# Kernel optimization log

Hardware: AMD Instinct MI355X
Metric: run time of the kernel (lower is better)

The kernel has to match this reference:

```python
import jax, jax.numpy as jnp
import numpy as np

N = 512       # num_nodes (feature dim of x == num_nodes, per GCNConv(num_nodes, f1))
BZ = 32       # subjects
TC = 256      # tc_length
F1 = 256
F2 = 128
E = 524288    # edges in the given (corr) graph over all bz*N nodes
NTOT = BZ * N
SLOPE = 0.2   # leaky relu negative_slope


def setup_inputs() -> dict:
    key = jax.random.key(0)
    ks = jax.random.split(key, 17)
    w = lambda k, shape: (jax.random.normal(k, shape, jnp.float32) * (shape[-1] ** -0.5))
    return {
        "x": jax.random.normal(ks[0], (NTOT, N), jnp.float32),
        "t": jax.random.normal(ks[1], (NTOT, TC), jnp.float32),
        "gumbel_u": jax.random.uniform(ks[2], (BZ, N, N, 2), jnp.float32),
        "edge_index": jax.random.randint(ks[3], (2, E), 0, NTOT, jnp.int64 if jax.config.jax_enable_x64 else jnp.int32),
        "conv1_w": w(ks[4], (F1, N)),
        "conv1_b": jnp.zeros((F1,), jnp.float32),
        "conv2_w": w(ks[5], (F2, F1)),
        "conv2_b": jnp.zeros((F2,), jnp.float32),
        "fc_cat_w": w(ks[6], (2, 2 * TC)),
        "fc_cat_b": jnp.zeros((2,), jnp.float32),
        "fcn1_w": w(ks[7], (256, F2 * 2 * N)),
        "fcn1_b": jnp.zeros((256,), jnp.float32),
        "fcn2_w": w(ks[8], (32, 256)),
        "fcn2_b": jnp.zeros((32,), jnp.float32),
        "fcn3_w": w(ks[9], (2, 32)),
        "fcn3_b": jnp.zeros((2,), jnp.float32),
    }


def _gcn_dense(x, A, W, b):
    # PyG GCNConv on a dense 0/1 adjacency A (edge r->c means A[r,c]=1):
    # add self loop, in-degree symmetric norm, aggregate sources into targets.
    n = A.shape[0]
    Ah = A + jnp.eye(n, dtype=A.dtype)
    deg = Ah.sum(axis=0)                                  # in-degree (targets = cols)
    dis = jnp.where(deg > 0, jax.lax.rsqrt(deg), 0.0)
    M = dis[:, None] * Ah * dis[None, :]                  # M[j,i] = d_j^-1/2 A_hat[j,i] d_i^-1/2
    return M.T @ (x @ W.T) + b


def _gcn_sparse(x, row, col, W, b):
    n = x.shape[0]
    loops = jnp.arange(n, dtype=row.dtype)
    r = jnp.concatenate([row, loops])
    c = jnp.concatenate([col, loops])
    deg = jax.ops.segment_sum(jnp.ones_like(c, x.dtype), c, num_segments=n)
    dis = jnp.where(deg > 0, jax.lax.rsqrt(deg), 0.0)
    norm = dis[r] * dis[c]                                # [E+n]
    xw = x @ W.T                                          # [n, out]
    out = jax.ops.segment_sum(xw[r] * norm[:, None], c, num_segments=n)
    return out + b


def reference(x, t, gumbel_u, edge_index, conv1_w, conv1_b, conv2_w, conv2_b,
              fc_cat_w, fc_cat_b, fcn1_w, fcn1_b, fcn2_w, fcn2_b, fcn3_w, fcn3_b):
    bz = t.shape[0] // N
    tb = t.reshape(bz, N, -1)
    xb = x.reshape(bz, N, -1)
    # fc_cat(relu(cat([senders, receivers]))) factors into per-node terms:
    Ws = fc_cat_w[:, :TC]   # multiplies senders half
    Wr = fc_cat_w[:, TC:]   # multiplies receivers half

    def per_sample(ti, xi, ui):
        u = jax.nn.relu(ti)                               # [N, TC]
        ls = u @ Ws.T                                     # [N, 2] sender term
        lr = u @ Wr.T                                     # [N, 2] receiver term
        # pair k = i*N+j has receiver t_i, sender t_j
        logits = lr[:, None, :] + ls[None, :, :] + fc_cat_b   # [N, N, 2]
        g = -jnp.log(-jnp.log(jnp.clip(ui, 1e-9, 1.0 - 1e-9)))  # Gumbel(0,1)
        y = logits + g                                    # tau = 1
        A = (jnp.argmax(y, axis=-1) == 0).astype(xi.dtype)    # hard sample, class 0 => edge
        A = jax.lax.stop_gradient(A)                      # torch.where -> indices blocks grad
        h = jax.nn.relu(_gcn_dense(xi, A, conv1_w, conv1_b))
        return _gcn_dense(h, A, conv2_w, conv2_b)         # [N, F2]

    x_op = jax.vmap(per_sample)(tb, xb, gumbel_u)         # [bz, N, F2]

    row, col = edge_index[0], edge_index[1]
    x_corr = jax.nn.relu(_gcn_sparse(x, row, col, conv1_w, conv1_b))
    x_corr = _gcn_sparse(x_corr, row, col, conv2_w, conv2_b)   # [bz*N, F2]

    emb = jnp.concatenate([x_op.reshape(-1, F2), x_corr], axis=1)  # [bz*N, 2*F2]
    emb = emb.reshape(bz, -1)                             # [bz, 2*F2*N]
    h = jax.nn.leaky_relu(emb @ fcn1_w.T + fcn1_b, SLOPE)
    h = jax.nn.leaky_relu(h @ fcn2_w.T + fcn2_b, SLOPE)
    return h @ fcn3_w.T + fcn3_b                          # [bz, 2]
```

## Files before the change

### kernel.cpp

```cpp
#include <hip/hip_runtime.h>
#include <hip/hip_bf16.h>

typedef __bf16 bf16_t;
typedef __bf16 bf16x8 __attribute__((ext_vector_type(8)));
typedef __bf16 bf16x4 __attribute__((ext_vector_type(4)));
typedef float f32x4 __attribute__((ext_vector_type(4)));

constexpr int kN = 512;
constexpr int kBZ = 32;
constexpr int kTC = 256;
constexpr int kE = 524288;
constexpr int kNTOT = 16384;

__global__ __launch_bounds__(256) void k_cvt3(const float* __restrict__ x, const float* __restrict__ c1w,
                                              const float* __restrict__ c2w, bf16_t* __restrict__ xb,
                                              bf16_t* __restrict__ c1b, bf16_t* __restrict__ c2b,
                                              int* __restrict__ counts) {
    int i = blockIdx.x * 256 + threadIdx.x;
    const int n0 = 2097152, n1 = n0 + 32768, n2 = n1 + 8192, n3 = n2 + 4096;
    if (i < n0) {
        float4 v = ((const float4*)x)[i];
        bf16x4 o = {(bf16_t)v.x, (bf16_t)v.y, (bf16_t)v.z, (bf16_t)v.w};
        ((bf16x4*)xb)[i] = o;
    } else if (i < n1) {
        int j = i - n0;
        float4 v = ((const float4*)c1w)[j];
        bf16x4 o = {(bf16_t)v.x, (bf16_t)v.y, (bf16_t)v.z, (bf16_t)v.w};
        ((bf16x4*)c1b)[j] = o;
    } else if (i < n2) {
        int j = i - n1;
        float4 v = ((const float4*)c2w)[j];
        bf16x4 o = {(bf16_t)v.x, (bf16_t)v.y, (bf16_t)v.z, (bf16_t)v.w};
        ((bf16x4*)c2b)[j] = o;
    } else if (i < n3) {
        int j = i - n2;
        ((int4*)counts)[j] = make_int4(0, 0, 0, 0);
    }
}

__global__ __launch_bounds__(256) void k_lsr(const float* __restrict__ tin, const float* __restrict__ fcw,
                                             const float* __restrict__ fcb, float4* __restrict__ lsr) {
    int row = blockIdx.x * 4 + (threadIdx.x >> 6);
    int lane = threadIdx.x & 63;
    const float* tr = tin + (size_t)row * kTC;
    float s0 = 0, s1 = 0, r0 = 0, r1 = 0;
    for (int k = lane; k < kTC; k += 64) {
        float u = fmaxf(tr[k], 0.f);
        s0 += u * fcw[k];
        s1 += u * fcw[512 + k];
        r0 += u * fcw[256 + k];
        r1 += u * fcw[768 + k];
    }
#pragma unroll
    for (int off = 32; off > 0; off >>= 1) {
        s0 += __shfl_down(s0, off); s1 += __shfl_down(s1, off);
        r0 += __shfl_down(r0, off); r1 += __shfl_down(r1, off);
    }
    if (lane == 0) lsr[row] = make_float4(s0 + fcb[0], s1 + fcb[1], r0, r1);
}

__global__ __launch_bounds__(256) void k_adj(const float* __restrict__ gum, const float4* __restrict__ lsr,
                                             bf16_t* __restrict__ AT) {
    int s = blockIdx.z;
    int a0 = blockIdx.y * 64, b0 = blockIdx.x * 64;
    __shared__ bf16_t tile[64][72];
    int t = threadIdx.x;
    int lb = t & 63, ra = t >> 6;
    int b = b0 + lb;
    float4 pb = lsr[s * kN + b];
#pragma unroll 4
    for (int p = 0; p < 16; p++) {
        int a = a0 + p * 4 + ra;
        float4 qa = lsr[s * kN + a];
        const float* g = gum + ((((size_t)s * kN + a) * kN + b) << 1);
        float u0 = fmaxf(g[0], 1e-9f);
        float u1 = fmaxf(g[1], 1e-9f);
        float g0 = -__logf(-__logf(u0));
        float g1 = -__logf(-__logf(u1));
        float v = ((qa.z + pb.x + g0) >= (qa.w + pb.y + g1)) ? 1.f : 0.f;
        if (a == b) v += 1.f;
        tile[lb][p * 4 + ra] = (bf16_t)v;
    }
    __syncthreads();
    int rj = t >> 3, li = (t & 7) * 8;
#pragma unroll
    for (int p = 0; p < 2; p++) {
        int j = p * 32 + rj;
        *(bf16x8*)(AT + ((size_t)s * kN + b0 + j) * kN + a0 + li) = *(const bf16x8*)&tile[j][li];
    }
}

__global__ __launch_bounds__(256) void k_degdis(const bf16_t* __restrict__ AT, float* __restrict__ dis) {
    int row = blockIdx.x * 4 + (threadIdx.x >> 6);
    int lane = threadIdx.x & 63;
    bf16x8 v = *(const bf16x8*)(AT + (size_t)row * kN + lane * 8);
    float s = 0;
#pragma unroll
    for (int i = 0; i < 8; i++) s += (float)v[i];
#pragma unroll
    for (int off = 32; off > 0; off >>= 1) s += __shfl_down(s, off);
    if (lane == 0) dis[row] = rsqrtf(s);
}

template <int MODE>
__global__ __launch_bounds__(256) void k_gemm(const bf16_t* __restrict__ A, const bf16_t* __restrict__ B,
                                              bf16_t* __restrict__ C, int K, int lda, int ldb, int ldc,
                                              size_t sA, size_t sB, size_t sC,
                                              const float* __restrict__ scale, const float* __restrict__ bias) {
    int m0 = blockIdx.x * 128, n0 = blockIdx.y * 128, s = blockIdx.z;
    A += sA * s; B += sB * s; C += sC * s;
    __shared__ bf16_t As[128][72], Bs[128][72];
    f32x4 acc[4][4] = {};
    int tid = threadIdx.x;
    int wave = tid >> 6, lane = tid & 63;
    int wm = (wave & 1) * 64, wn = (wave >> 1) * 64;
    int fm = lane & 15, fq = lane >> 4;
    int srow = tid >> 3, scol = (tid & 7) * 8;
    for (int kb = 0; kb < K; kb += 64) {
        __syncthreads();
#pragma unroll
        for (int p = 0; p < 4; p++) {
            int row = p * 32 + srow;
            *(uint4*)&As[row][scol] = *(const uint4*)(A + (size_t)(m0 + row) * lda + kb + scol);
            *(uint4*)&Bs[row][scol] = *(const uint4*)(B + (size_t)(n0 + row) * ldb + kb + scol);
        }
        __syncthreads();
#pragma unroll
        for (int kk = 0; kk < 2; kk++) {
            bf16x8 af[4], bfr[4];
#pragma unroll
            for (int i = 0; i < 4; i++) {
                af[i] = *(const bf16x8*)&As[wm + i * 16 + fm][kk * 32 + fq * 8];
                bfr[i] = *(const bf16x8*)&Bs[wn + i * 16 + fm][kk * 32 + fq * 8];
            }
#pragma unroll
            for (int i = 0; i < 4; i++)
#pragma unroll
                for (int j = 0; j < 4; j++)
                    acc[i][j] = __builtin_amdgcn_mfma_f32_16x16x32_bf16(af[i], bfr[j], acc[i][j], 0, 0, 0);
        }
    }
#pragma unroll
    for (int i = 0; i < 4; i++) {
#pragma unroll
        for (int r = 0; r < 4; r++) {
            int row = wm + i * 16 + fq * 4 + r;
            float sc = 1.f;
            if constexpr (MODE != 0) sc = scale[(size_t)s * kN + m0 + row];
#pragma unroll
            for (int j = 0; j < 4; j++) {
                int col = n0 + wn + j * 16 + fm;
                float v = acc[i][j][r];
                if constexpr (MODE == 1) v = fmaxf(sc * v + bias[col], 0.f);
                if constexpr (MODE == 2) v = sc * v + bias[col];
                C[(size_t)(m0 + row) * ldc + col] = (bf16_t)v;
            }
        }
    }
}

template <int F>
__global__ __launch_bounds__(256) void k_scaleT(const bf16_t* __restrict__ XW, const float* __restrict__ dis,
                                                bf16_t* __restrict__ ZT) {
    int s = blockIdx.z, i0 = blockIdx.y * 64, f0 = blockIdx.x * 64;
    __shared__ bf16_t tile[64][72];
    int t = threadIdx.x;
    int gi = t >> 3, gc = (t & 7) * 8;
#pragma unroll
    for (int p = 0; p < 2; p++) {
        int i = p * 32 + gi;
        bf16x8 v = *(const bf16x8*)(XW + (size_t)(s * kN + i0 + i) * F + f0 + gc);
        float d = dis[s * kN + i0 + i];
#pragma unroll
        for (int q = 0; q < 8; q++) tile[gc + q][i] = (bf16_t)(d * (float)v[q]);
    }
    __syncthreads();
#pragma unroll
    for (int p = 0; p < 2; p++) {
        int f = p * 32 + gi;
        *(bf16x8*)(ZT + (size_t)(s * F + f0 + f) * kN + i0 + gc) = *(const bf16x8*)&tile[f][gc];
    }
}


__global__ __launch_bounds__(256) void k_hist(const int* __restrict__ col, int* __restrict__ counts) {
    int e = blockIdx.x * 256 + threadIdx.x;
    if (e < kE) atomicAdd(&counts[col[e]], 1);
}

__global__ __launch_bounds__(256) void k_scan(const int* __restrict__ counts, int* __restrict__ offsets,
                                              int* __restrict__ cursor, float* __restrict__ dis_s) {
    __shared__ int ldc_[16384];
    __shared__ int sums[256];
    int t = threadIdx.x;
    for (int i = 0; i < 64; i++) {
        int g = i * 256 + t;
        int c = counts[g];
        ldc_[g] = c;
        dis_s[g] = rsqrtf((float)(c + 1));
    }
    __syncthreads();
    int s = 0;
    for (int i = 0; i < 64; i++) s += ldc_[t * 64 + i];
    sums[t] = s;
    __syncthreads();
    for (int off = 1; off < 256; off <<= 1) {
        int y = (t >= off) ? sums[t - off] : 0;
        __syncthreads();
        sums[t] += y;
        __syncthreads();
    }
    int run = sums[t] - s;
    for (int i = 0; i < 64; i++) {
        int j = t * 64 + i;
        int c = ldc_[j];
        ldc_[j] = run;
        run += c;
    }
    __syncthreads();
    for (int i = 0; i < 64; i++) {
        int g = i * 256 + t;
        int o = ldc_[g];
        offsets[g] = o;
        cursor[g] = o;
    }
}

__global__ __launch_bounds__(256) void k_fill(const int* __restrict__ row, const int* __restrict__ col,
                                              int* __restrict__ cursor, int* __restrict__ list) {
    int e = blockIdx.x * 256 + threadIdx.x;
    if (e < kE) {
        int p = atomicAdd(&cursor[col[e]], 1);
        list[p] = row[e];
    }
}

template <int F, bool RELU>
__global__ __launch_bounds__(256) void k_sagg(const bf16_t* __restrict__ XW, int rowOffIn,
                                              const int* __restrict__ list, const int* __restrict__ offsets,
                                              const int* __restrict__ counts, const float* __restrict__ dis_s,
                                              const float* __restrict__ bias, bf16_t* __restrict__ OUT,
                                              int outColOff) {
    constexpr int TPR = F / 8;
    constexpr int RPB = 256 / TPR;
    int j = blockIdx.x * RPB + threadIdx.x / TPR;
    int f8 = (threadIdx.x % TPR) * 8;
    float dj = dis_s[j];
    const bf16_t* base = XW + (size_t)rowOffIn * F;
    float acc[8];
    {
        bf16x8 v = *(const bf16x8*)(base + (size_t)j * F + f8);
#pragma unroll
        for (int q = 0; q < 8; q++) acc[q] = dj * (float)v[q];
    }
    int off = offsets[j], cnt = counts[j];
    int e = 0;
    for (; e + 4 <= cnt; e += 4) {
        int r0 = list[off + e], r1 = list[off + e + 1], r2 = list[off + e + 2], r3 = list[off + e + 3];
        float d0 = dis_s[r0], d1 = dis_s[r1], d2 = dis_s[r2], d3 = dis_s[r3];
        bf16x8 v0 = *(const bf16x8*)(base + (size_t)r0 * F + f8);
        bf16x8 v1 = *(const bf16x8*)(base + (size_t)r1 * F + f8);
        bf16x8 v2 = *(const bf16x8*)(base + (size_t)r2 * F + f8);
        bf16x8 v3 = *(const bf16x8*)(base + (size_t)r3 * F + f8);
#pragma unroll
        for (int q = 0; q < 8; q++)
            acc[q] += (d0 * (float)v0[q] + d1 * (float)v1[q]) + (d2 * (float)v2[q] + d3 * (float)v3[q]);
    }
    for (; e < cnt; e++) {
        int r = list[off + e];
        float d = dis_s[r];
        bf16x8 v = *(const bf16x8*)(base + (size_t)r * F + f8);
#pragma unroll
        for (int q = 0; q < 8; q++) acc[q] += d * (float)v[q];
    }
    bf16x8 o;
#pragma unroll
    for (int q = 0; q < 8; q++) {
        float v = dj * acc[q] + bias[f8 + q];
        if (RELU) v = fmaxf(v, 0.f);
        o[q] = (bf16_t)v;
    }
    *(bf16x8*)(OUT + (size_t)j * 256 + outColOff + f8) = o;
}

__global__ __launch_bounds__(256) void k_fcn1(const bf16_t* __restrict__ EMB, const float* __restrict__ W1,
                                              float* __restrict__ partials) {
    int tid = threadIdx.x, wave = tid >> 6, lane = tid & 63;
    int fm = lane & 15, fq = lane >> 4;
    int kb0 = blockIdx.x * 256;
    f32x4 acc[2][4] = {};
#pragma unroll 2
    for (int ks = 0; ks < 256; ks += 32) {
        int k = kb0 + ks + fq * 8;
        bf16x8 a0 = *(const bf16x8*)(EMB + (size_t)fm * 131072 + k);
        bf16x8 a1 = *(const bf16x8*)(EMB + (size_t)(16 + fm) * 131072 + k);
        bf16x8 bfr[4];
#pragma unroll
        for (int j = 0; j < 4; j++) {
            int n = wave * 64 + j * 16 + fm;
            const float* p = W1 + (size_t)n * 131072 + k;
            float4 lo = *(const float4*)p;
            float4 hi = *(const float4*)(p + 4);
            bf16x8 b = {(bf16_t)lo.x, (bf16_t)lo.y, (bf16_t)lo.z, (bf16_t)lo.w,
                        (bf16_t)hi.x, (bf16_t)hi.y, (bf16_t)hi.z, (bf16_t)hi.w};
            bfr[j] = b;
        }
#pragma unroll
        for (int j = 0; j < 4; j++) {
            acc[0][j] = __builtin_amdgcn_mfma_f32_16x16x32_bf16(a0, bfr[j], acc[0][j], 0, 0, 0);
            acc[1][j] = __builtin_amdgcn_mfma_f32_16x16x32_bf16(a1, bfr[j], acc[1][j], 0, 0, 0);
        }
    }
    float* P = partials + (size_t)blockIdx.x * 8192;
#pragma unroll
    for (int i = 0; i < 2; i++)
#pragma unroll
        for (int j = 0; j < 4; j++)
#pragma unroll
            for (int r = 0; r < 4; r++)
                P[(size_t)(i * 16 + fq * 4 + r) * 256 + wave * 64 + j * 16 + fm] = acc[i][j][r];
}

__global__ __launch_bounds__(256) void k_reduce(const float* __restrict__ partials, float* __restrict__ part2) {
    int kg = blockIdx.x >> 5, eb = blockIdx.x & 31;
    int e = eb * 256 + threadIdx.x;
    float s = 0;
#pragma unroll 8
    for (int i = 0; i < 64; i++) s += partials[(size_t)(kg * 64 + i) * 8192 + e];
    part2[(size_t)kg * 8192 + e] = s;
}

__global__ __launch_bounds__(256) void k_head(const float* __restrict__ part2, const float* __restrict__ b1,
                                              const float* __restrict__ W2, const float* __restrict__ b2,
                                              const float* __restrict__ W3, const float* __restrict__ b3,
                                              float* __restrict__ out) {
    __shared__ float h1s[32][256];
    __shared__ float h2s[32][32];
    int t = threadIdx.x;
    for (int i = 0; i < 32; i++) {
        int e = i * 256 + t;
        float s = 0;
#pragma unroll
        for (int kg = 0; kg < 8; kg++) s += part2[kg * 8192 + e];
        s += b1[t];
        h1s[i][t] = (s > 0.f) ? s : 0.2f * s;
    }
    __syncthreads();
    for (int p = 0; p < 4; p++) {
        int id = p * 256 + t, si = id >> 5, o2 = id & 31;
        float s = 0;
        for (int k = 0; k < 256; k++) s += h1s[si][k] * W2[o2 * 256 + k];
        s += b2[o2];
        h2s[si][o2] = (s > 0.f) ? s : 0.2f * s;
    }
    __syncthreads();
    if (t < 64) {
        int si = t >> 1, o3 = t & 1;
        float s = 0;
#pragma unroll
        for (int k = 0; k < 32; k++) s += h2s[si][k] * W3[o3 * 32 + k];
        out[si * 2 + o3] = s + b3[o3];
    }
}


extern "C" void kernel_launch(void* const* d_in, const int* in_sizes, int n_in,
                              void* d_out, int out_size, void* d_ws, size_t ws_size,
                              hipStream_t stream) {
    const float* x = (const float*)d_in[0];
    const float* t = (const float*)d_in[1];
    const float* gum = (const float*)d_in[2];
    const int* eidx = (const int*)d_in[3];
    const float* c1w = (const float*)d_in[4];
    const float* c1b = (const float*)d_in[5];
    const float* c2w = (const float*)d_in[6];
    const float* c2b = (const float*)d_in[7];
    const float* fcw = (const float*)d_in[8];
    const float* fcb = (const float*)d_in[9];
    const float* w1 = (const float*)d_in[10];
    const float* b1 = (const float*)d_in[11];
    const float* w2 = (const float*)d_in[12];
    const float* b2 = (const float*)d_in[13];
    const float* w3 = (const float*)d_in[14];
    const float* b3 = (const float*)d_in[15];
    float* out = (float*)d_out;
    (void)in_sizes; (void)n_in; (void)out_size; (void)ws_size;

    char* ws = (char*)d_ws;
    size_t off = 0;
    auto alloc = [&](size_t bytes) -> char* {
        char* p = ws + off;
        off += (bytes + 255) & ~size_t(255);
        return p;
    };
    bf16_t* xbf_H = (bf16_t*)alloc((size_t)32768 * 256 * 2);
    bf16_t* c1wb = (bf16_t*)alloc((size_t)256 * 512 * 2);
    bf16_t* c2wb = (bf16_t*)alloc((size_t)128 * 256 * 2);
    float4* lsr = (float4*)alloc((size_t)kNTOT * 16);
    bf16_t* AT = (bf16_t*)alloc((size_t)kBZ * kN * kN * 2);
    float* disd = (float*)alloc((size_t)kNTOT * 4);
    bf16_t* XW1_EMB = (bf16_t*)alloc((size_t)kNTOT * 256 * 2);
    bf16_t* Z1T = (bf16_t*)alloc((size_t)kBZ * 256 * 512 * 2);
    bf16_t* XW2 = (bf16_t*)alloc((size_t)32768 * 128 * 2);
    bf16_t* Z2T = (bf16_t*)alloc((size_t)kBZ * 128 * 512 * 2);
    int* counts = (int*)alloc((size_t)kNTOT * 4);
    int* offsets = (int*)alloc((size_t)kNTOT * 4);
    int* cursor = (int*)alloc((size_t)kNTOT * 4);
    float* diss = (float*)alloc((size_t)kNTOT * 4);
    int* list = (int*)alloc((size_t)kE * 4);
    float* part2 = (float*)alloc((size_t)8 * 8192 * 4);

    bf16_t* xbf = xbf_H;
    bf16_t* H = xbf_H;
    bf16_t* XW1 = XW1_EMB;
    bf16_t* EMB = XW1_EMB;
    float* partials = (float*)AT;

    k_cvt3<<<8368, 256, 0, stream>>>(x, c1w, c2w, xbf, c1wb, c2wb, counts);
    k_lsr<<<4096, 256, 0, stream>>>(t, fcw, fcb, lsr);
    k_adj<<<dim3(8, 8, 32), 256, 0, stream>>>(gum, lsr, AT);
    k_degdis<<<4096, 256, 0, stream>>>(AT, disd);
    k_gemm<0><<<dim3(128, 2, 1), 256, 0, stream>>>(xbf, c1wb, XW1, 512, 512, 512, 256, 0, 0, 0, nullptr, nullptr);
    k_hist<<<2048, 256, 0, stream>>>(eidx + kE, counts);
    k_scan<<<1, 256, 0, stream>>>(counts, offsets, cursor, diss);
    k_fill<<<2048, 256, 0, stream>>>(eidx, eidx + kE, cursor, list);
    k_scaleT<256><<<dim3(4, 8, 32), 256, 0, stream>>>(XW1, disd, Z1T);
    k_gemm<1><<<dim3(4, 2, 32), 256, 0, stream>>>(AT, Z1T, H, 512, 512, 512, 256,
                                                  (size_t)512 * 512, (size_t)256 * 512, (size_t)512 * 256, disd, c1b);
    k_sagg<256, true><<<2048, 256, 0, stream>>>(XW1, 0, list, offsets, counts, diss, c1b,
                                                H + (size_t)16384 * 256, 0);
    k_gemm<0><<<dim3(256, 1, 1), 256, 0, stream>>>(H, c2wb, XW2, 256, 256, 256, 128, 0, 0, 0, nullptr, nullptr);
    k_scaleT<128><<<dim3(2, 8, 32), 256, 0, stream>>>(XW2, disd, Z2T);
    k_gemm<2><<<dim3(4, 1, 32), 256, 0, stream>>>(AT, Z2T, EMB, 512, 512, 512, 256,
                                                  (size_t)512 * 512, (size_t)128 * 512, (size_t)512 * 256, disd, c2b);
    k_sagg<128, false><<<1024, 256, 0, stream>>>(XW2, 16384, list, offsets, counts, diss, c2b, EMB, 128);
    k_fcn1<<<512, 256, 0, stream>>>(EMB, w1, partials);
    k_reduce<<<256, 256, 0, stream>>>(partials, part2);
    k_head<<<1, 256, 0, stream>>>(part2, b1, w2, b2, w3, b3, out);
}
```

Measured before the change: 521.7 us.

## Fuse conversions, degree reduction and scale-transpose into adjacent kernels; split fcn1 finer

The x-to-bf16 conversion is folded into the first projection GEMM, which now reads fp32 directly. The dense-graph degree sum moves into the adjacency kernel via atomics. The separate scale-transpose kernels are folded into the GEMM epilogue, which writes both XW and the degree-scaled transposed Z. The scan's shared array is padded to avoid bank conflicts, and the fcn1 K-split doubles its block count with a separate partials buffer instead of aliasing AT. This removes several kernel launches and intermediate round trips, at the cost of atomics and a heavier GEMM epilogue.

```diff
diff --git a/kernel.cpp b/kernel.cpp
--- a/kernel.cpp
+++ b/kernel.cpp
@@ -12,29 +12,24 @@
 constexpr int kE = 524288;
 constexpr int kNTOT = 16384;
 
-__global__ __launch_bounds__(256) void k_cvt3(const float* __restrict__ x, const float* __restrict__ c1w,
-                                              const float* __restrict__ c2w, bf16_t* __restrict__ xb,
+__global__ __launch_bounds__(256) void k_cvt3(const float* __restrict__ c1w, const float* __restrict__ c2w,
                                               bf16_t* __restrict__ c1b, bf16_t* __restrict__ c2b,
-                                              int* __restrict__ counts) {
+                                              int* __restrict__ counts, float* __restrict__ degsum) {
     int i = blockIdx.x * 256 + threadIdx.x;
-    const int n0 = 2097152, n1 = n0 + 32768, n2 = n1 + 8192, n3 = n2 + 4096;
+    const int n0 = 32768, n1 = n0 + 8192, n2 = n1 + 4096, n3 = n2 + 4096;
     if (i < n0) {
-        float4 v = ((const float4*)x)[i];
+        float4 v = ((const float4*)c1w)[i];
         bf16x4 o = {(bf16_t)v.x, (bf16_t)v.y, (bf16_t)v.z, (bf16_t)v.w};
-        ((bf16x4*)xb)[i] = o;
+        ((bf16x4*)c1b)[i] = o;
     } else if (i < n1) {
         int j = i - n0;
-        float4 v = ((const float4*)c1w)[j];
-        bf16x4 o = {(bf16_t)v.x, (bf16_t)v.y, (bf16_t)v.z, (bf16_t)v.w};
-        ((bf16x4*)c1b)[j] = o;
-    } else if (i < n2) {
-        int j = i - n1;
         float4 v = ((const float4*)c2w)[j];
         bf16x4 o = {(bf16_t)v.x, (bf16_t)v.y, (bf16_t)v.z, (bf16_t)v.w};
         ((bf16x4*)c2b)[j] = o;
+    } else if (i < n2) {
+        ((int4*)counts)[i - n1] = make_int4(0, 0, 0, 0);
     } else if (i < n3) {
-        int j = i - n2;
-        ((int4*)counts)[j] = make_int4(0, 0, 0, 0);
+        ((float4*)degsum)[i - n2] = make_float4(0.f, 0.f, 0.f, 0.f);
     }
 }
 
@@ -60,7 +55,7 @@
 }
 
 __global__ __launch_bounds__(256) void k_adj(const float* __restrict__ gum, const float4* __restrict__ lsr,
-                                             bf16_t* __restrict__ AT) {
+                                             bf16_t* __restrict__ AT, float* __restrict__ degsum) {
     int s = blockIdx.z;
     int a0 = blockIdx.y * 64, b0 = blockIdx.x * 64;
     __shared__ bf16_t tile[64][72];
@@ -86,27 +81,23 @@
 #pragma unroll
     for (int p = 0; p < 2; p++) {
         int j = p * 32 + rj;
-        *(bf16x8*)(AT + ((size_t)s * kN + b0 + j) * kN + a0 + li) = *(const bf16x8*)&tile[j][li];
-    }
-}
-
-__global__ __launch_bounds__(256) void k_degdis(const bf16_t* __restrict__ AT, float* __restrict__ dis) {
-    int row = blockIdx.x * 4 + (threadIdx.x >> 6);
-    int lane = threadIdx.x & 63;
-    bf16x8 v = *(const bf16x8*)(AT + (size_t)row * kN + lane * 8);
-    float s = 0;
-#pragma unroll
-    for (int i = 0; i < 8; i++) s += (float)v[i];
-#pragma unroll
-    for (int off = 32; off > 0; off >>= 1) s += __shfl_down(s, off);
-    if (lane == 0) dis[row] = rsqrtf(s);
+        bf16x8 v = *(const bf16x8*)&tile[j][li];
+        *(bf16x8*)(AT + ((size_t)s * kN + b0 + j) * kN + a0 + li) = v;
+        float ps = 0;
+#pragma unroll
+        for (int q = 0; q < 8; q++) ps += (float)v[q];
+        ps += __shfl_down(ps, 4);
+        ps += __shfl_down(ps, 2);
+        ps += __shfl_down(ps, 1);
+        if ((t & 7) == 0) atomicAdd(degsum + s * kN + b0 + j, ps);
+    }
 }
 
 template <int MODE>
 __global__ __launch_bounds__(256) void k_gemm(const bf16_t* __restrict__ A, const bf16_t* __restrict__ B,
                                               bf16_t* __restrict__ C, int K, int lda, int ldb, int ldc,
                                               size_t sA, size_t sB, size_t sC,
-                                              const float* __restrict__ scale, const float* __restrict__ bias) {
+                                              const float* __restrict__ degsum, const float* __restrict__ bias) {
     int m0 = blockIdx.x * 128, n0 = blockIdx.y * 128, s = blockIdx.z;
     A += sA * s; B += sB * s; C += sC * s;
     __shared__ bf16_t As[128][72], Bs[128][72];
@@ -145,40 +136,90 @@
 #pragma unroll
         for (int r = 0; r < 4; r++) {
             int row = wm + i * 16 + fq * 4 + r;
-            float sc = 1.f;
-            if constexpr (MODE != 0) sc = scale[(size_t)s * kN + m0 + row];
+            float sc = rsqrtf(degsum[(size_t)s * kN + m0 + row]);
 #pragma unroll
             for (int j = 0; j < 4; j++) {
                 int col = n0 + wn + j * 16 + fm;
-                float v = acc[i][j][r];
-                if constexpr (MODE == 1) v = fmaxf(sc * v + bias[col], 0.f);
-                if constexpr (MODE == 2) v = sc * v + bias[col];
+                float v = sc * acc[i][j][r] + bias[col];
+                if constexpr (MODE == 1) v = fmaxf(v, 0.f);
                 C[(size_t)(m0 + row) * ldc + col] = (bf16_t)v;
             }
         }
     }
 }
 
-template <int F>
-__global__ __launch_bounds__(256) void k_scaleT(const bf16_t* __restrict__ XW, const float* __restrict__ dis,
-                                                bf16_t* __restrict__ ZT) {
-    int s = blockIdx.z, i0 = blockIdx.y * 64, f0 = blockIdx.x * 64;
-    __shared__ bf16_t tile[64][72];
-    int t = threadIdx.x;
-    int gi = t >> 3, gc = (t & 7) * 8;
-#pragma unroll
-    for (int p = 0; p < 2; p++) {
-        int i = p * 32 + gi;
-        bf16x8 v = *(const bf16x8*)(XW + (size_t)(s * kN + i0 + i) * F + f0 + gc);
-        float d = dis[s * kN + i0 + i];
-#pragma unroll
-        for (int q = 0; q < 8; q++) tile[gc + q][i] = (bf16_t)(d * (float)v[q]);
-    }
-    __syncthreads();
-#pragma unroll
-    for (int p = 0; p < 2; p++) {
-        int f = p * 32 + gi;
-        *(bf16x8*)(ZT + (size_t)(s * F + f0 + f) * kN + i0 + gc) = *(const bf16x8*)&tile[f][gc];
+template <bool AF32, int F, int DENSE_ROWS>
+__global__ __launch_bounds__(256) void k_gemmT(const void* __restrict__ Ap, const bf16_t* __restrict__ B,
+                                               bf16_t* __restrict__ XW, bf16_t* __restrict__ ZT, int K,
+                                               const float* __restrict__ degsum) {
+    int m0 = blockIdx.x * 128, n0 = blockIdx.y * 128;
+    __shared__ __align__(16) bf16_t smem[2 * 128 * 72];
+    bf16_t* AsBase = smem;
+    bf16_t* BsBase = smem + 128 * 72;
+    f32x4 acc[4][4] = {};
+    int tid = threadIdx.x;
+    int wave = tid >> 6, lane = tid & 63;
+    int wm = (wave & 1) * 64, wn = (wave >> 1) * 64;
+    int fm = lane & 15, fq = lane >> 4;
+    int srow = tid >> 3, scol = (tid & 7) * 8;
+    for (int kb = 0; kb < K; kb += 64) {
+        __syncthreads();
+#pragma unroll
+        for (int p = 0; p < 4; p++) {
+            int row = p * 32 + srow;
+            if constexpr (AF32) {
+                const float* ap = (const float*)Ap + (size_t)(m0 + row) * K + kb + scol;
+                float4 lo = *(const float4*)ap;
+                float4 hi = *(const float4*)(ap + 4);
+                bf16x8 o = {(bf16_t)lo.x, (bf16_t)lo.y, (bf16_t)lo.z, (bf16_t)lo.w,
+                            (bf16_t)hi.x, (bf16_t)hi.y, (bf16_t)hi.z, (bf16_t)hi.w};
+                *(bf16x8*)&AsBase[row * 72 + scol] = o;
+            } else {
+                *(uint4*)&AsBase[row * 72 + scol] =
+                    *(const uint4*)((const bf16_t*)Ap + (size_t)(m0 + row) * K + kb + scol);
+            }
+            *(uint4*)&BsBase[row * 72 + scol] = *(const uint4*)(B + (size_t)(n0 + row) * K + kb + scol);
+        }
+        __syncthreads();
+#pragma unroll
+        for (int kk = 0; kk < 2; kk++) {
+            bf16x8 af[4], bfr[4];
+#pragma unroll
+            for (int i = 0; i < 4; i++) {
+                af[i] = *(const bf16x8*)&AsBase[(wm + i * 16 + fm) * 72 + kk * 32 + fq * 8];
+                bfr[i] = *(const bf16x8*)&BsBase[(wn + i * 16 + fm) * 72 + kk * 32 + fq * 8];
+            }
+#pragma unroll
+            for (int i = 0; i < 4; i++)
+#pragma unroll
+                for (int j = 0; j < 4; j++)
+                    acc[i][j] = __builtin_amdgcn_mfma_f32_16x16x32_bf16(af[i], bfr[j], acc[i][j], 0, 0, 0);
+        }
+    }
+    bool doT = (m0 < DENSE_ROWS);
+    __syncthreads();
+#pragma unroll
+    for (int i = 0; i < 4; i++) {
+#pragma unroll
+        for (int r = 0; r < 4; r++) {
+            int row = wm + i * 16 + fq * 4 + r;
+            float sc = doT ? rsqrtf(degsum[m0 + row]) : 0.f;
+#pragma unroll
+            for (int j = 0; j < 4; j++) {
+                int col = wn + j * 16 + fm;
+                float v = acc[i][j][r];
+                XW[(size_t)(m0 + row) * F + n0 + col] = (bf16_t)v;
+                if (doT) smem[col * 136 + row] = (bf16_t)(sc * v);
+            }
+        }
+    }
+    if (doT) {
+        __syncthreads();
+        int fr = tid >> 1, hi = (tid & 1) * 64;
+        bf16_t* zrow = ZT + ((size_t)(m0 >> 9) * F + n0 + fr) * kN + (m0 & 511) + hi;
+#pragma unroll
+        for (int q = 0; q < 8; q++)
+            *(bf16x8*)(zrow + q * 8) = *(const bf16x8*)&smem[fr * 136 + hi + q * 8];
     }
 }
 
@@ -190,18 +231,19 @@
 
 __global__ __launch_bounds__(256) void k_scan(const int* __restrict__ counts, int* __restrict__ offsets,
                                               int* __restrict__ cursor, float* __restrict__ dis_s) {
-    __shared__ int ldc_[16384];
+    __shared__ int ldc_[16896];
     __shared__ int sums[256];
     int t = threadIdx.x;
+#define IDX(j) ((j) + ((j) >> 5))
     for (int i = 0; i < 64; i++) {
         int g = i * 256 + t;
         int c = counts[g];
-        ldc_[g] = c;
+        ldc_[IDX(g)] = c;
         dis_s[g] = rsqrtf((float)(c + 1));
     }
     __syncthreads();
     int s = 0;
-    for (int i = 0; i < 64; i++) s += ldc_[t * 64 + i];
+    for (int i = 0; i < 64; i++) s += ldc_[IDX(t * 64 + i)];
     sums[t] = s;
     __syncthreads();
     for (int off = 1; off < 256; off <<= 1) {
@@ -213,17 +255,18 @@
     int run = sums[t] - s;
     for (int i = 0; i < 64; i++) {
         int j = t * 64 + i;
-        int c = ldc_[j];
-        ldc_[j] = run;
+        int c = ldc_[IDX(j)];
+        ldc_[IDX(j)] = run;
         run += c;
     }
     __syncthreads();
     for (int i = 0; i < 64; i++) {
         int g = i * 256 + t;
-        int o = ldc_[g];
+        int o = ldc_[IDX(g)];
         offsets[g] = o;
         cursor[g] = o;
     }
+#undef IDX
 }
 
 __global__ __launch_bounds__(256) void k_fill(const int* __restrict__ row, const int* __restrict__ col,
@@ -287,10 +330,10 @@
                                               float* __restrict__ partials) {
     int tid = threadIdx.x, wave = tid >> 6, lane = tid & 63;
     int fm = lane & 15, fq = lane >> 4;
-    int kb0 = blockIdx.x * 256;
+    int kb0 = blockIdx.x * 128;
     f32x4 acc[2][4] = {};
-#pragma unroll 2
-    for (int ks = 0; ks < 256; ks += 32) {
+#pragma unroll
+    for (int ks = 0; ks < 128; ks += 32) {
         int k = kb0 + ks + fq * 8;
         bf16x8 a0 = *(const bf16x8*)(EMB + (size_t)fm * 131072 + k);
         bf16x8 a1 = *(const bf16x8*)(EMB + (size_t)(16 + fm) * 131072 + k);
@@ -326,7 +369,7 @@
     int e = eb * 256 + threadIdx.x;
     float s = 0;
 #pragma unroll 8
-    for (int i = 0; i < 64; i++) s += partials[(size_t)(kg * 64 + i) * 8192 + e];
+    for (int i = 0; i < 128; i++) s += partials[(size_t)(kg * 128 + i) * 8192 + e];
     part2[(size_t)kg * 8192 + e] = s;
 }
 
@@ -393,14 +436,14 @@
         off += (bytes + 255) & ~size_t(255);
         return p;
     };
-    bf16_t* xbf_H = (bf16_t*)alloc((size_t)32768 * 256 * 2);
     bf16_t* c1wb = (bf16_t*)alloc((size_t)256 * 512 * 2);
     bf16_t* c2wb = (bf16_t*)alloc((size_t)128 * 256 * 2);
     float4* lsr = (float4*)alloc((size_t)kNTOT * 16);
     bf16_t* AT = (bf16_t*)alloc((size_t)kBZ * kN * kN * 2);
-    float* disd = (float*)alloc((size_t)kNTOT * 4);
+    float* degsum = (float*)alloc((size_t)kNTOT * 4);
     bf16_t* XW1_EMB = (bf16_t*)alloc((size_t)kNTOT * 256 * 2);
     bf16_t* Z1T = (bf16_t*)alloc((size_t)kBZ * 256 * 512 * 2);
+    bf16_t* H = (bf16_t*)alloc((size_t)32768 * 256 * 2);
     bf16_t* XW2 = (bf16_t*)alloc((size_t)32768 * 128 * 2);
     bf16_t* Z2T = (bf16_t*)alloc((size_t)kBZ * 128 * 512 * 2);
     int* counts = (int*)alloc((size_t)kNTOT * 4);
@@ -408,33 +451,30 @@
     int* cursor = (int*)alloc((size_t)kNTOT * 4);
     float* diss = (float*)alloc((size_t)kNTOT * 4);
     int* list = (int*)alloc((size_t)kE * 4);
+    float* partials = (float*)alloc((size_t)1024 * 8192 * 4);
     float* part2 = (float*)alloc((size_t)8 * 8192 * 4);
 
-    bf16_t* xbf = xbf_H;
-    bf16_t* H = xbf_H;
     bf16_t* XW1 = XW1_EMB;
     bf16_t* EMB = XW1_EMB;
-    float* partials = (float*)AT;
-
-    k_cvt3<<<8368, 256, 0, stream>>>(x, c1w, c2w, xbf, c1wb, c2wb, counts);
+
+    k_cvt3<<<192, 256, 0, stream>>>(c1w, c2w, c1wb, c2wb, counts, degsum);
     k_lsr<<<4096, 256, 0, stream>>>(t, fcw, fcb, lsr);
-    k_adj<<<dim3(8, 8, 32), 256, 0, stream>>>(gum, lsr, AT);
-    k_degdis<<<4096, 256, 0, stream>>>(AT, disd);
-    k_gemm<0><<<dim3(128, 2, 1), 256, 0, stream>>>(xbf, c1wb, XW1, 512, 512, 512, 256, 0, 0, 0, nullptr, nullptr);
+    k_adj<<<dim3(8, 8, 32), 256, 0, stream>>>(gum, lsr, AT, degsum);
     k_hist<<<2048, 256, 0, stream>>>(eidx + kE, counts);
     k_scan<<<1, 256, 0, stream>>>(counts, offsets, cursor, diss);
     k_fill<<<2048, 256, 0, stream>>>(eidx, eidx + kE, cursor, list);
-    k_scaleT<256><<<dim3(4, 8, 32), 256, 0, stream>>>(XW1, disd, Z1T);
+    k_gemmT<true, 256, kNTOT><<<dim3(128, 2, 1), 256, 0, stream>>>(x, c1wb, XW1, Z1T, 512, degsum);
     k_gemm<1><<<dim3(4, 2, 32), 256, 0, stream>>>(AT, Z1T, H, 512, 512, 512, 256,
-                                                  (size_t)512 * 512, (size_t)256 * 512, (size_t)512 * 256, disd, c1b);
+                                                  (size_t)512 * 512, (size_t)256 * 512, (size_t)512 * 256,
+                                                  degsum, c1b);
     k_sagg<256, true><<<2048, 256, 0, stream>>>(XW1, 0, list, offsets, counts, diss, c1b,
                                                 H + (size_t)16384 * 256, 0);
-    k_gemm<0><<<dim3(256, 1, 1), 256, 0, stream>>>(H, c2wb, XW2, 256, 256, 256, 128, 0, 0, 0, nullptr, nullptr);
-    k_scaleT<128><<<dim3(2, 8, 32), 256, 0, stream>>>(XW2, disd, Z2T);
+    k_gemmT<false, 128, kNTOT><<<dim3(256, 1, 1), 256, 0, stream>>>(H, c2wb, XW2, Z2T, 256, degsum);
     k_gemm<2><<<dim3(4, 1, 32), 256, 0, stream>>>(AT, Z2T, EMB, 512, 512, 512, 256,
-                                                  (size_t)512 * 512, (size_t)128 * 512, (size_t)512 * 256, disd, c2b);
+                                                  (size_t)512 * 512, (size_t)128 * 512, (size_t)512 * 256,
+                                                  degsum, c2b);
     k_sagg<128, false><<<1024, 256, 0, stream>>>(XW2, 16384, list, offsets, counts, diss, c2b, EMB, 128);
-    k_fcn1<<<512, 256, 0, stream>>>(EMB, w1, partials);
+    k_fcn1<<<1024, 256, 0, stream>>>(EMB, w1, partials);
     k_reduce<<<256, 256, 0, stream>>>(partials, part2);
     k_head<<<1, 256, 0, stream>>>(part2, b1, w2, b2, w3, b3, out);
 }
```

After: 517.3 us. Within noise of the previous version (-0.8%).
